# Kernel tuning notes

Measured on AMD Instinct MI355X. Metric: run time of the kernel, lower is better.

The kernel has to match this reference:

```python
import jax, jax.numpy as jnp
import numpy as np

UNITS = 1024
OUT_STEPS = 200
SEQ_LEN = 5
NUM_FEATURES = 1
BATCH = 4096


def _lstm_cell(x, h, c, kernel, recurrent_kernel, bias):
    # Keras LSTMCell: z = x@K + h@R + b, gates in order i, f, g(candidate), o
    z = x @ kernel + h @ recurrent_kernel + bias  # [B, 4U]
    i, f, g, o = jnp.split(z, 4, axis=-1)
    i = jax.nn.sigmoid(i)
    f = jax.nn.sigmoid(f)
    g = jnp.tanh(g)
    o = jax.nn.sigmoid(o)
    c_new = f * c + i * g
    h_new = o * jnp.tanh(c_new)
    return h_new, c_new


def setup_inputs() -> dict:
    key = jax.random.key(0)
    ks = jax.random.split(key, 8)
    s = 0.05  # modest init scale to keep gates unsaturated
    return {
        "inputs": jax.random.normal(ks[0], (BATCH, SEQ_LEN, NUM_FEATURES), jnp.float32),
        "kernel": jax.random.normal(ks[1], (NUM_FEATURES, 4 * UNITS), jnp.float32) * s,
        "recurrent_kernel": jax.random.normal(ks[2], (UNITS, 4 * UNITS), jnp.float32) * s,
        "bias": jax.random.normal(ks[3], (4 * UNITS,), jnp.float32) * s,
        "w1": jax.random.normal(ks[4], (UNITS, NUM_FEATURES), jnp.float32) * s,
        "b1": jax.random.normal(ks[5], (NUM_FEATURES,), jnp.float32) * s,
        "w2": jax.random.normal(ks[6], (NUM_FEATURES, NUM_FEATURES), jnp.float32) * s,
        "b2": jax.random.normal(ks[7], (NUM_FEATURES,), jnp.float32) * s,
    }


def reference(inputs, kernel, recurrent_kernel, bias, w1, b1, w2, b2):
    B = inputs.shape[0]
    h0 = jnp.zeros((B, UNITS), inputs.dtype)
    c0 = jnp.zeros((B, UNITS), inputs.dtype)

    # warmup: run LSTM over the input sequence (lax.scan over time)
    def warm_step(carry, x_t):
        h, c = carry
        h, c = _lstm_cell(x_t, h, c, kernel, recurrent_kernel, bias)
        return (h, c), None

    (h, c), _ = jax.lax.scan(warm_step, (h0, c0), jnp.swapaxes(inputs, 0, 1))
    pred0 = jax.nn.relu(h @ w1 + b1)  # first prediction: dense1 only (per warmup())

    def dec_step(carry, _):
        pred, h, c = carry
        h, c = _lstm_cell(pred, h, c, kernel, recurrent_kernel, bias)
        x = jax.nn.relu(h @ w1 + b1)
        pred = x @ w2 + b2
        return (pred, h, c), pred

    _, preds = jax.lax.scan(dec_step, (pred0, h, c), None, length=OUT_STEPS - 1)
    # preds: [T-1, B, F] -> stack with pred0 and transpose to [B, T, F]
    all_preds = jnp.concatenate([pred0[None], preds], axis=0)
    return jnp.transpose(all_preds, (1, 0, 2))
```

## Files before the change

kernel.cpp:

```cpp
#include <hip/hip_runtime.h>
#include <hip/hip_bf16.h>
#include <stdint.h>
#include <stddef.h>

#define B_SZ   4096
#define U_SZ   1024
#define SEQ    5
#define TSTEPS 200
#define STEPS  204

typedef __bf16 bf16_t;
typedef __bf16 bf16x8 __attribute__((ext_vector_type(8)));
typedef float  f32x4  __attribute__((ext_vector_type(4)));

#define AS1 __attribute__((address_space(1)))
#define AS3 __attribute__((address_space(3)))

#define LOAD_LDS16(gp, lp) \
    __builtin_amdgcn_global_load_lds((const AS1 unsigned int*)(gp), \
                                     (AS3 unsigned int*)(lp), 16, 0, 0)

__device__ __forceinline__ float fsig(float x) {
    return 1.0f / (1.0f + __expf(-x));
}
__device__ __forceinline__ float ftanh(float x) {
    x = fminf(fmaxf(x, -15.0f), 15.0f);
    float e = __expf(2.0f * x);
    return (e - 1.0f) / (e + 1.0f);
}

__global__ void pack_R(const float* __restrict__ R, bf16_t* __restrict__ Rp) {
    int idx = blockIdx.x * 256 + threadIdx.x;
    int e    = idx & 7;
    int slot = (idx >> 3) & 7;
    int c    = (idx >> 6) & 127;
    int kb   = (idx >> 13) & 15;
    int ub   = idx >> 17;
    int g  = (c >> 4) & 3;
    int wc = c >> 6;
    int cl = c & 15;
    int n  = g * 1024 + ub * 32 + wc * 16 + cl;
    int k  = kb * 64 + ((slot ^ (c & 7)) << 3) + e;
    Rp[idx] = (bf16_t)R[(size_t)k * 4096 + n];
}

__global__ __launch_bounds__(256, 2)
void lstm_step(const bf16_t* __restrict__ hin,
               bf16_t* __restrict__ hout,
               float* __restrict__ cst,
               const bf16_t* __restrict__ Rp,
               const float* __restrict__ Wx,
               const float* __restrict__ bias,
               const float* __restrict__ w1,
               const float* __restrict__ b1,
               const float* __restrict__ w2,
               const float* __restrict__ b2,
               const float* __restrict__ inputs,
               float* __restrict__ praw,
               float* __restrict__ out,
               int t)
{
    __shared__ __align__(16) bf16_t lsA[128 * 64];
    __shared__ __align__(16) bf16_t lsB[2][128 * 64];
    __shared__ float lsX[128];

    const int tid  = threadIdx.x;
    const int wave = tid >> 6;
    const int lane = tid & 63;
    const int p    = blockIdx.x;
    const int G    = blockIdx.y;
    const int l15  = lane & 15;
    const int quad = lane >> 4;
    const int rbase = (wave >> 1) * 64;
    const int wc    = wave & 1;

    float*       pr_acc  = praw + (size_t)(t % 3) * B_SZ;
    const float* pr_read = praw + (size_t)((t + 2) % 3) * B_SZ;
    float*       pr_zero = praw + (size_t)((t + 1) % 3) * B_SZ;

    if (tid < 128) {
        int row = G * 128 + tid;
        float x;
        if (t < SEQ) {
            x = inputs[row * SEQ + t];
        } else {
            float x1 = fmaxf(pr_read[row] + b1[0], 0.f);
            x = (t == SEQ) ? x1 : x1 * w2[0] + b2[0];
            if (p == 0) out[(size_t)row * TSTEPS + (t - SEQ)] = x;
        }
        lsX[tid] = x;
        if (p == 0) pr_zero[row] = 0.f;
    }

    f32x4 acc[2][4][4] = {};
    const bf16_t* Ap  = hin + (size_t)G * 128 * U_SZ;
    const bf16_t* Bp0 = Rp + (size_t)(2 * p) * 131072;
    const bf16_t* Bp1 = Bp0 + 131072;

    const int a_kk = (((lane & 7) ^ (lane >> 3)) << 3);

    for (int kb = 0; kb < 16; ++kb) {
        #pragma unroll
        for (int i = 0; i < 4; ++i) {
            int chunk = wave * 4 + i;
            int m  = chunk * 8 + (lane >> 3);
            LOAD_LDS16(Ap + (size_t)m * U_SZ + kb * 64 + a_kk, &lsA[chunk * 512]);
        }
        #pragma unroll
        for (int i = 0; i < 4; ++i) {
            int chunk = wave * 4 + i;
            LOAD_LDS16(Bp0 + (size_t)kb * 8192 + chunk * 512 + lane * 8,
                       &lsB[0][chunk * 512]);
            LOAD_LDS16(Bp1 + (size_t)kb * 8192 + chunk * 512 + lane * 8,
                       &lsB[1][chunk * 512]);
        }
        __syncthreads();

        #pragma unroll
        for (int kh = 0; kh < 2; ++kh) {
            int sw = (((kh * 4 + quad) ^ (lane & 7)) << 3);
            bf16x8 af[4];
            #pragma unroll
            for (int mi = 0; mi < 4; ++mi)
                af[mi] = *(const bf16x8*)&lsA[(rbase + mi * 16 + l15) * 64 + sw];
            #pragma unroll
            for (int T = 0; T < 2; ++T) {
                bf16x8 bfr[4];
                #pragma unroll
                for (int ni = 0; ni < 4; ++ni)
                    bfr[ni] = *(const bf16x8*)
                        &lsB[T][(wc * 64 + ni * 16 + l15) * 64 + sw];
                #pragma unroll
                for (int mi = 0; mi < 4; ++mi)
                    #pragma unroll
                    for (int ni = 0; ni < 4; ++ni)
                        acc[T][mi][ni] = __builtin_amdgcn_mfma_f32_16x16x32_bf16(
                            af[mi], bfr[ni], acc[T][mi][ni], 0, 0, 0);
            }
        }
        __syncthreads();
    }

    int uu[2];
    uu[0] = (2 * p) * 32 + wc * 16 + l15;
    uu[1] = uu[0] + 32;
    float g_b[2][4], g_w[2][4], w1u[2];
    #pragma unroll
    for (int T = 0; T < 2; ++T) {
        #pragma unroll
        for (int g = 0; g < 4; ++g) {
            g_b[T][g] = bias[g * 1024 + uu[T]];
            g_w[T][g] = Wx[g * 1024 + uu[T]];
        }
        w1u[T] = w1[uu[T]];
    }
    const bool do_pred = (t >= SEQ - 1);

    #pragma unroll
    for (int mi = 0; mi < 4; ++mi) {
        #pragma unroll
        for (int r = 0; r < 4; ++r) {
            int rl   = rbase + mi * 16 + quad * 4 + r;
            int brow = G * 128 + rl;
            float xv = lsX[rl];
            float ps = 0.f;
            #pragma unroll
            for (int T = 0; T < 2; ++T) {
                float zi = acc[T][mi][0][r] + g_b[T][0] + xv * g_w[T][0];
                float zf = acc[T][mi][1][r] + g_b[T][1] + xv * g_w[T][1];
                float zg = acc[T][mi][2][r] + g_b[T][2] + xv * g_w[T][2];
                float zo = acc[T][mi][3][r] + g_b[T][3] + xv * g_w[T][3];
                float ig = fsig(zi), fg = fsig(zf);
                float gg = ftanh(zg), og = fsig(zo);
                size_t off = (size_t)brow * U_SZ + uu[T];
                float cn = fg * cst[off] + ig * gg;
                cst[off] = cn;
                float hv = og * ftanh(cn);
                hout[off] = (bf16_t)hv;
                ps += hv * w1u[T];
            }
            if (do_pred) {
                ps += __shfl_xor(ps, 1);
                ps += __shfl_xor(ps, 2);
                ps += __shfl_xor(ps, 4);
                ps += __shfl_xor(ps, 8);
                if (l15 == 0) atomicAdd(&pr_acc[brow], ps);
            }
        }
    }
}

__global__ void pred_final(const float* __restrict__ praw,
                           const float* __restrict__ b1,
                           const float* __restrict__ w2,
                           const float* __restrict__ b2,
                           float* __restrict__ out)
{
    int row = blockIdx.x * 256 + threadIdx.x;
    float x1 = fmaxf(praw[2 * B_SZ + row] + b1[0], 0.f);
    out[(size_t)row * TSTEPS + 199] = x1 * w2[0] + b2[0];
}

extern "C" void kernel_launch(void* const* d_in, const int* in_sizes, int n_in,
                              void* d_out, int out_size, void* d_ws, size_t ws_size,
                              hipStream_t stream) {
    const float* inputs = (const float*)d_in[0];
    const float* Wx     = (const float*)d_in[1];
    const float* R      = (const float*)d_in[2];
    const float* bias   = (const float*)d_in[3];
    const float* w1     = (const float*)d_in[4];
    const float* b1     = (const float*)d_in[5];
    const float* w2     = (const float*)d_in[6];
    const float* b2     = (const float*)d_in[7];
    float* out = (float*)d_out;

    char* ws = (char*)d_ws;
    const size_t RP_BYTES = (size_t)32 * 131072 * 2;
    const size_t H_BYTES  = (size_t)B_SZ * U_SZ * 2;
    const size_t C_BYTES  = (size_t)B_SZ * U_SZ * 4;
    bf16_t* Rp   = (bf16_t*)ws;                ws += RP_BYTES;
    bf16_t* h0   = (bf16_t*)ws;                ws += H_BYTES;
    bf16_t* h1   = (bf16_t*)ws;                ws += H_BYTES;
    float*  cbuf = (float*)ws;                 ws += C_BYTES;
    float*  praw = (float*)ws;                 ws += 3 * B_SZ * 4;
    bf16_t* hb[2] = {h0, h1};

    hipMemsetAsync(h0, 0, H_BYTES, stream);
    hipMemsetAsync(cbuf, 0, C_BYTES, stream);
    hipMemsetAsync(praw, 0, 3 * B_SZ * 4, stream);

    pack_R<<<16384, 256, 0, stream>>>(R, Rp);

    dim3 grid(16, 32);
    int cur = 0;
    for (int t = 0; t < STEPS; ++t) {
        lstm_step<<<grid, 256, 0, stream>>>(hb[cur], hb[1 - cur], cbuf, Rp,
                                            Wx, bias, w1, b1, w2, b2,
                                            inputs, praw, out, t);
        cur ^= 1;
    }
    pred_final<<<16, 256, 0, stream>>>(praw, b1, w2, b2, out);
}
```

Before: 8.692 ms.

## Load h fragments directly to registers and double-buffer recurrent weights in LDS

The recurrent GEMM's k-loop is restructured so the h (A) fragments are read straight from global memory into registers, software-pipelined one half-block ahead, and no longer staged through LDS. The packed R tiles (B) are double-buffered in LDS: the next k-block is prefetched while the current one feeds the MFMAs. A manual waitcnt plus a single barrier per iteration replaces the two __syncthreads, and s_setprio raises wave priority around the MFMA bursts. The aim is to hide global load latency and cut barrier stalls. In exchange, LDS use per block grows and the code relies on hand-counted vmcnt ordering.

```diff
diff --git a/kernel.cpp b/kernel.cpp
--- a/kernel.cpp
+++ b/kernel.cpp
@@ -60,8 +60,7 @@
                float* __restrict__ out,
                int t)
 {
-    __shared__ __align__(16) bf16_t lsA[128 * 64];
-    __shared__ __align__(16) bf16_t lsB[2][128 * 64];
+    __shared__ __align__(16) bf16_t lsB[2][2][8192];
     __shared__ float lsX[128];
 
     const int tid  = threadIdx.x;
@@ -78,6 +77,11 @@
     const float* pr_read = praw + (size_t)((t + 2) % 3) * B_SZ;
     float*       pr_zero = praw + (size_t)((t + 1) % 3) * B_SZ;
 
+    const bf16_t* Ap  = hin + (size_t)G * 128 * U_SZ;
+    const bf16_t* Bp0 = Rp + (size_t)(2 * p) * 131072;
+    const bf16_t* Bp1 = Bp0 + 131072;
+    const bf16_t* Arow = Ap + (size_t)(rbase + l15) * U_SZ + quad * 8;
+
     if (tid < 128) {
         int row = G * 128 + tid;
         float x;
@@ -92,53 +96,87 @@
         if (p == 0) pr_zero[row] = 0.f;
     }
 
-    f32x4 acc[2][4][4] = {};
-    const bf16_t* Ap  = hin + (size_t)G * 128 * U_SZ;
-    const bf16_t* Bp0 = Rp + (size_t)(2 * p) * 131072;
-    const bf16_t* Bp1 = Bp0 + 131072;
-
-    const int a_kk = (((lane & 7) ^ (lane >> 3)) << 3);
-
-    for (int kb = 0; kb < 16; ++kb) {
+    auto STAGE_B = [&](int ksrc, int par) {
         #pragma unroll
         for (int i = 0; i < 4; ++i) {
             int chunk = wave * 4 + i;
-            int m  = chunk * 8 + (lane >> 3);
-            LOAD_LDS16(Ap + (size_t)m * U_SZ + kb * 64 + a_kk, &lsA[chunk * 512]);
-        }
-        #pragma unroll
-        for (int i = 0; i < 4; ++i) {
-            int chunk = wave * 4 + i;
-            LOAD_LDS16(Bp0 + (size_t)kb * 8192 + chunk * 512 + lane * 8,
-                       &lsB[0][chunk * 512]);
-            LOAD_LDS16(Bp1 + (size_t)kb * 8192 + chunk * 512 + lane * 8,
-                       &lsB[1][chunk * 512]);
-        }
-        __syncthreads();
-
-        #pragma unroll
-        for (int kh = 0; kh < 2; ++kh) {
-            int sw = (((kh * 4 + quad) ^ (lane & 7)) << 3);
-            bf16x8 af[4];
-            #pragma unroll
-            for (int mi = 0; mi < 4; ++mi)
-                af[mi] = *(const bf16x8*)&lsA[(rbase + mi * 16 + l15) * 64 + sw];
-            #pragma unroll
-            for (int T = 0; T < 2; ++T) {
-                bf16x8 bfr[4];
+            LOAD_LDS16(Bp0 + (size_t)ksrc * 8192 + chunk * 512 + lane * 8,
+                       &lsB[par][0][chunk * 512]);
+            LOAD_LDS16(Bp1 + (size_t)ksrc * 8192 + chunk * 512 + lane * 8,
+                       &lsB[par][1][chunk * 512]);
+        }
+    };
+
+    STAGE_B(0, 0);
+    bf16x8 afA[4], afB[4];
+    #pragma unroll
+    for (int mi = 0; mi < 4; ++mi)
+        afA[mi] = *(const bf16x8*)(Arow + (size_t)mi * 16 * U_SZ);
+
+    f32x4 acc[2][4][4] = {};
+
+    #pragma clang loop unroll(disable)
+    for (int kb = 0; kb < 16; ++kb) {
+        asm volatile("s_waitcnt vmcnt(4) lgkmcnt(0)" ::: "memory");
+        __builtin_amdgcn_sched_barrier(0);
+        __builtin_amdgcn_s_barrier();
+        __builtin_amdgcn_sched_barrier(0);
+
+        if (kb < 15) STAGE_B(kb + 1, (kb + 1) & 1);
+
+        #pragma unroll
+        for (int mi = 0; mi < 4; ++mi)
+            afB[mi] = *(const bf16x8*)(Arow + (size_t)mi * 16 * U_SZ
+                                            + kb * 64 + 32);
+
+        const bf16_t* lb = &lsB[kb & 1][0][0];
+
+        {
+            const int sw = ((quad ^ (lane & 7)) << 3);
+            bf16x8 bfr[2][4];
+            #pragma unroll
+            for (int T = 0; T < 2; ++T)
                 #pragma unroll
                 for (int ni = 0; ni < 4; ++ni)
-                    bfr[ni] = *(const bf16x8*)
-                        &lsB[T][(wc * 64 + ni * 16 + l15) * 64 + sw];
+                    bfr[T][ni] = *(const bf16x8*)
+                        &lb[T * 8192 + (wc * 64 + ni * 16 + l15) * 64 + sw];
+            __builtin_amdgcn_s_setprio(1);
+            #pragma unroll
+            for (int T = 0; T < 2; ++T)
                 #pragma unroll
                 for (int mi = 0; mi < 4; ++mi)
                     #pragma unroll
                     for (int ni = 0; ni < 4; ++ni)
                         acc[T][mi][ni] = __builtin_amdgcn_mfma_f32_16x16x32_bf16(
-                            af[mi], bfr[ni], acc[T][mi][ni], 0, 0, 0);
-            }
-        }
-        __syncthreads();
+                            afA[mi], bfr[T][ni], acc[T][mi][ni], 0, 0, 0);
+            __builtin_amdgcn_s_setprio(0);
+        }
+
+        #pragma unroll
+        for (int mi = 0; mi < 4; ++mi)
+            afA[mi] = *(const bf16x8*)(Arow + (size_t)mi * 16 * U_SZ
+                                            + ((kb + 1) & 15) * 64);
+
+        {
+            const int sw = (((4 + quad) ^ (lane & 7)) << 3);
+            bf16x8 bfr[2][4];
+            #pragma unroll
+            for (int T = 0; T < 2; ++T)
+                #pragma unroll
+                for (int ni = 0; ni < 4; ++ni)
+                    bfr[T][ni] = *(const bf16x8*)
+                        &lb[T * 8192 + (wc * 64 + ni * 16 + l15) * 64 + sw];
+            __builtin_amdgcn_s_setprio(1);
+            #pragma unroll
+            for (int T = 0; T < 2; ++T)
+                #pragma unroll
+                for (int mi = 0; mi < 4; ++mi)
+                    #pragma unroll
+                    for (int ni = 0; ni < 4; ++ni)
+                        acc[T][mi][ni] = __builtin_amdgcn_mfma_f32_16x16x32_bf16(
+                            afB[mi], bfr[T][ni], acc[T][mi][ni], 0, 0, 0);
+            __builtin_amdgcn_s_setprio(0);
+        }
     }
 
     int uu[2];
```

Result: slower. 11.42 ms (+31.4%).
